# Kernel optimization log

Hardware: AMD Instinct MI355X
Metric: run time of the kernel (lower is better)

The kernel has to match this reference:

```python
import jax, jax.numpy as jnp
import numpy as np

NUM_GENES = 50000
NUM_EDGES = 5000
NNZ = 1_600_000
NUM_PATHWAYS = 500
NUM_TREATMENTS = 20
D = 128        # embed_dim
LATENT = 128   # latent_dim
B, M = 64, 200


def setup_inputs() -> dict:
    key = jax.random.key(0)
    ks = jax.random.split(key, 14)
    gene_ids = jax.random.randint(ks[0], (B, M), 0, NUM_GENES)
    context_ids = jax.random.randint(ks[1], (B,), 0, NUM_TREATMENTS)
    # sparse incidence H (COO): H[row, col] = val, shape [NUM_GENES, NUM_EDGES]
    H_rows = jax.random.randint(ks[2], (NNZ,), 0, NUM_GENES)
    H_cols = jax.random.randint(ks[3], (NNZ,), 0, NUM_EDGES)
    H_vals = jnp.ones((NNZ,), jnp.float32)
    gene_embed = 0.02 * jax.random.normal(ks[4], (NUM_GENES, D), jnp.float32)
    treatment_embed = 0.02 * jax.random.normal(ks[5], (NUM_TREATMENTS, D), jnp.float32)
    gene_pathway = jax.random.bernoulli(ks[6], 0.05, (NUM_GENES, NUM_PATHWAYS)).astype(jnp.float32)
    s = 1.0 / np.sqrt(2 * D)
    W1 = s * jax.random.normal(ks[7], (2 * D, D), jnp.float32)
    b1 = jnp.zeros((D,), jnp.float32)
    W2 = (1.0 / np.sqrt(D)) * jax.random.normal(ks[8], (D,), jnp.float32)
    b2 = jnp.zeros((), jnp.float32)
    latent_W = (1.0 / np.sqrt(D)) * jax.random.normal(ks[9], (D, LATENT), jnp.float32)
    latent_b = jnp.zeros((LATENT,), jnp.float32)
    risk_W = (1.0 / np.sqrt(LATENT)) * jax.random.normal(ks[10], (LATENT,), jnp.float32)
    risk_b = jnp.zeros((), jnp.float32)
    return dict(gene_ids=gene_ids, context_ids=context_ids, H_rows=H_rows, H_cols=H_cols,
                H_vals=H_vals, gene_embed=gene_embed, treatment_embed=treatment_embed,
                gene_pathway=gene_pathway, W1=W1, b1=b1, W2=W2, b2=b2,
                latent_W=latent_W, latent_b=latent_b, risk_W=risk_W, risk_b=risk_b)


def _hyper_prop(E, H_rows, H_cols, H_vals):
    Dv = jax.ops.segment_sum(H_vals, H_rows, num_segments=NUM_GENES)
    De = jax.ops.segment_sum(H_vals, H_cols, num_segments=NUM_EDGES)
    dv = jnp.power(Dv + 1e-6, -0.5)[:, None]   # [V,1]
    de = jnp.power(De + 1e-6, -1.0)[:, None]   # [E,1]
    X = E * dv
    # H^T X : scatter node rows into hyperedges
    HX = jax.ops.segment_sum(H_vals[:, None] * X[H_rows], H_cols, num_segments=NUM_EDGES)
    HX = HX * de
    # H (De^-1 H^T X)
    Xp = jax.ops.segment_sum(H_vals[:, None] * HX[H_cols], H_rows, num_segments=NUM_GENES)
    return Xp * dv


def reference(gene_ids, context_ids, H_rows, H_cols, H_vals, gene_embed, treatment_embed,
              gene_pathway, W1, b1, W2, b2, latent_W, latent_b, risk_W, risk_b):
    E_prop = _hyper_prop(gene_embed, H_rows, H_cols, H_vals)   # [V,D]
    X = E_prop[gene_ids]                                       # [B,M,D]
    ctx = treatment_embed[context_ids]                         # [B,D]
    masks = gene_pathway[gene_ids]                             # [B,M,P]
    pathway_sum = jnp.einsum('bmd,bmp->bpd', X, masks)         # [B,P,D]
    counts = jnp.clip(masks.sum(axis=1), 1.0)[..., None]       # [B,P,1]
    rep = pathway_sum / counts                                 # [B,P,D]
    ctx_exp = jnp.broadcast_to(ctx[:, None, :], (rep.shape[0], NUM_PATHWAYS, D))
    attn_in = jnp.concatenate([rep, ctx_exp], axis=-1)         # [B,P,2D]
    h = jnp.tanh(attn_in @ W1 + b1)                            # [B,P,D]
    scores = h @ W2 + b2                                       # [B,P]
    w = jax.nn.softmax(scores, axis=-1)
    z0 = jnp.einsum('bp,bpd->bd', w, rep)                      # [B,D]
    z = z0 @ latent_W + latent_b                               # [B,LATENT]
    risk = z @ risk_W + risk_b                                 # [B]
    return risk, z
```

## Files before the change

kernel.cpp:

```cpp
#include <hip/hip_runtime.h>
#include <math.h>

#define NGENES 50000
#define NEDGES 5000
#define NNZ_C 1600000
#define NPATH 500
#define DIM 128
#define BB 64
#define MM 200
#define BMN (BB * MM)
#define NBMW 1568
#define CSRCAP 400000
#define NCH 32
#define RNG 12512
#define GSTRIDE 50048
#define NT 8
#define TILESZ 6250
#define NBIN (NT * NEDGES)
#define BIN0 50048
#define EDGE0 90048
#define RED_N 95048
#define SCB_BIN 40
#define SCB_ROW 49
#define SCB (SCB_BIN + SCB_ROW)

__device__ inline float wred_sum(float x) {
#pragma unroll
  for (int off = 32; off > 0; off >>= 1) x += __shfl_down(x, off, 64);
  return x;
}
__device__ inline int wred_sumi(int x) {
#pragma unroll
  for (int off = 32; off > 0; off >>= 1) x += __shfl_down(x, off, 64);
  return x;
}
__device__ inline float wred_max(float x) {
#pragma unroll
  for (int off = 32; off > 0; off >>= 1) x = fmaxf(x, __shfl_down(x, off, 64));
  return x;
}
__device__ inline int wave_incl_scan(int x) {
  int lane = threadIdx.x & 63;
#pragma unroll
  for (int off = 1; off < 64; off <<= 1) {
    int y = __shfl_up(x, off, 64);
    if (lane >= off) x += y;
  }
  return x;
}

__global__ void k_mark(const int* __restrict__ gene_ids, unsigned* __restrict__ bitmap) {
  int i = blockIdx.x * blockDim.x + threadIdx.x;
  if (i >= BMN) return;
  int g = gene_ids[i];
  atomicOr(bitmap + (g >> 5), 1u << (g & 31));
}

__global__ void k_build(const int* __restrict__ rows, const int* __restrict__ cols,
                        const float* __restrict__ vals, const unsigned* __restrict__ bitmap,
                        float* __restrict__ pdv, int* __restrict__ pcnt,
                        int* __restrict__ pbc, float* __restrict__ pde) {
  __shared__ char smem_raw[60000];
  int c = blockIdx.x, role = blockIdx.y, tid = threadIdx.x;
  int lo = c * (NNZ_C / NCH), hi = lo + (NNZ_C / NCH);
  if (role < 4) {
    float* hs = (float*)smem_raw;
    int rlo = role * RNG;
    for (int j = tid; j < RNG; j += 1024) hs[j] = 0.f;
    __syncthreads();
    for (int i = lo + tid; i < hi; i += 1024) {
      int r = rows[i];
      unsigned d = (unsigned)(r - rlo);
      if (d < RNG) atomicAdd(&hs[d], vals[i]);
    }
    __syncthreads();
    float* dst = pdv + (size_t)c * GSTRIDE + rlo;
    for (int j = tid; j < RNG; j += 1024) dst[j] = hs[j];
  } else if (role < 8) {
    int* hs = (int*)smem_raw;
    unsigned* bm = (unsigned*)(smem_raw + RNG * 4);
    int rlo = (role - 4) * RNG;
    for (int j = tid; j < RNG; j += 1024) hs[j] = 0;
    for (int j = tid; j < NBMW; j += 1024) bm[j] = bitmap[j];
    __syncthreads();
    for (int i = lo + tid; i < hi; i += 1024) {
      int r = rows[i];
      unsigned d = (unsigned)(r - rlo);
      if (d < RNG && ((bm[r >> 5] >> (r & 31)) & 1)) atomicAdd(&hs[d], 1);
    }
    __syncthreads();
    int* dst = pcnt + (size_t)c * GSTRIDE + rlo;
    for (int j = tid; j < RNG; j += 1024) dst[j] = hs[j];
  } else {
    int p = role - 8;
    int* hc = (int*)smem_raw;
    float* hs = (float*)(smem_raw + 40000);
    for (int j = tid; j < 2 * NEDGES; j += 1024) hc[j] = 0;
    for (int j = tid; j < NEDGES; j += 1024) hs[j] = 0.f;
    __syncthreads();
    for (int i = lo + tid; i < hi; i += 1024) {
      int r = rows[i];
      int t = r / TILESZ;
      if ((t >> 1) != p) continue;
      int e = cols[i];
      atomicAdd(&hc[(t & 1) * NEDGES + e], 1);
      atomicAdd(&hs[e], vals[i]);
    }
    __syncthreads();
    for (int j = tid; j < 2 * NEDGES; j += 1024) {
      int h = j / NEDGES, e = j - h * NEDGES;
      pbc[(size_t)c * NBIN + (2 * p + h) * NEDGES + e] = hc[j];
    }
    for (int j = tid; j < NEDGES; j += 1024)
      pde[((size_t)c * 4 + p) * NEDGES + j] = hs[j];
  }
}

__global__ void k_reduce(const float* __restrict__ pdv, const int* __restrict__ pcnt,
                         const int* __restrict__ pbc, const float* __restrict__ pde,
                         float* __restrict__ dv_inv, int* __restrict__ row_cnt,
                         int* __restrict__ ccpre8, int* __restrict__ cnt8em,
                         float* __restrict__ de_inv) {
  int idx = blockIdx.x * 256 + threadIdx.x;
  if (idx < NGENES) {
    float s = 0.f;
    int n = 0;
    for (int c = 0; c < NCH; ++c) {
      s += pdv[(size_t)c * GSTRIDE + idx];
      n += pcnt[(size_t)c * GSTRIDE + idx];
    }
    dv_inv[idx] = 1.f / sqrtf(s + 1e-6f);
    row_cnt[idx] = n;
  } else if (idx >= BIN0 && idx < BIN0 + NBIN) {
    int b = idx - BIN0;
    int t = b / NEDGES, e = b - t * NEDGES;
    int run = 0;
    for (int c = 0; c < NCH; ++c) {
      ccpre8[(size_t)c * NBIN + b] = run;
      run += pbc[(size_t)c * NBIN + b];
    }
    cnt8em[(e << 3) | t] = run;
  } else if (idx >= EDGE0 && idx < EDGE0 + NEDGES) {
    int e = idx - EDGE0;
    float s = 0.f;
    for (int cp = 0; cp < NCH * 4; ++cp) s += pde[(size_t)cp * NEDGES + e];
    de_inv[e] = 1.f / (s + 1e-6f);
  }
}

__global__ void k_sc1(const int* __restrict__ cnt8em, const int* __restrict__ row_cnt,
                      int* __restrict__ bsum) {
  __shared__ int wsum[4];
  int blk = blockIdx.x, t = threadIdx.x, lane = t & 63, wid = t >> 6;
  const int* in;
  int base, n;
  if (blk < SCB_BIN) { in = cnt8em; base = blk * 1024; n = NBIN; }
  else { in = row_cnt; base = (blk - SCB_BIN) * 1024; n = NGENES; }
  int s = 0;
#pragma unroll
  for (int k = 0; k < 4; ++k) {
    int e = base + t + k * 256;
    if (e < n) s += in[e];
  }
  s = wred_sumi(s);
  if (lane == 0) wsum[wid] = s;
  __syncthreads();
  if (t == 0) bsum[blk] = wsum[0] + wsum[1] + wsum[2] + wsum[3];
}

__global__ void k_sc2(const int* __restrict__ bsum, int* __restrict__ boff) {
  int t = threadIdx.x, lane = t & 63, wid = t >> 6;
  if (wid == 0) {
    int x = (lane < SCB_BIN) ? bsum[lane] : 0;
    int incl = wave_incl_scan(x);
    if (lane < SCB_BIN) boff[lane] = incl - x;
  } else {
    int x = (lane < SCB_ROW) ? bsum[SCB_BIN + lane] : 0;
    int incl = wave_incl_scan(x);
    if (lane < SCB_ROW) boff[SCB_BIN + lane] = incl - x;
  }
}

__global__ void k_sc3(const int* __restrict__ cnt8em, const int* __restrict__ row_cnt,
                      const int* __restrict__ boff,
                      int* __restrict__ start8, int* __restrict__ row_start) {
  __shared__ int lds[1024];
  __shared__ int wsum[4];
  int blk = blockIdx.x, t = threadIdx.x, lane = t & 63, wid = t >> 6;
  const int* in;
  int* out;
  int base, n;
  if (blk < SCB_BIN) { in = cnt8em; out = start8; base = blk * 1024; n = NBIN; }
  else { in = row_cnt; out = row_start; base = (blk - SCB_BIN) * 1024; n = NGENES; }
  int coff = boff[blk];
#pragma unroll
  for (int k = 0; k < 4; ++k) {
    int e = t + k * 256;
    lds[e] = (base + e < n) ? in[base + e] : 0;
  }
  __syncthreads();
  int x0 = lds[4 * t], x1 = lds[4 * t + 1], x2 = lds[4 * t + 2], x3 = lds[4 * t + 3];
  int s = x0 + x1 + x2 + x3;
  int incl = wave_incl_scan(s);
  if (lane == 63) wsum[wid] = incl;
  __syncthreads();
  int woff = 0;
  for (int w = 0; w < wid; ++w) woff += wsum[w];
  int tb = coff + woff + incl - s;
  int i0 = base + 4 * t;
  if (i0 + 3 < n) {
    ((int4*)(out + i0))[0] = make_int4(tb, tb + x0, tb + x0 + x1, tb + x0 + x1 + x2);
  } else {
    if (i0 < n) out[i0] = tb;
    if (i0 + 1 < n) out[i0 + 1] = tb + x0;
    if (i0 + 2 < n) out[i0 + 2] = tb + x0 + x1;
    if (i0 + 3 < n) out[i0 + 3] = tb + x0 + x1 + x2;
  }
}

__global__ void k_place(const int* __restrict__ rows, const int* __restrict__ cols,
                        const float* __restrict__ vals, const float* __restrict__ dv_inv,
                        const int* __restrict__ start8, const int* __restrict__ ccpre8,
                        const int* __restrict__ row_start, int* __restrict__ row_cur,
                        const unsigned* __restrict__ bitmap,
                        int2* __restrict__ csc, int2* __restrict__ csr) {
  __shared__ char smem_raw[40000];
  int c = blockIdx.x, role = blockIdx.y, tid = threadIdx.x;
  int lo = c * (NNZ_C / NCH), hi = lo + (NNZ_C / NCH);
  if (role < 4) {
    int* cnt_s = (int*)smem_raw;
    for (int j = tid; j < 2 * NEDGES; j += 1024) cnt_s[j] = 0;
    __syncthreads();
    const int* cp = ccpre8 + (size_t)c * NBIN;
    for (int i = lo + tid; i < hi; i += 1024) {
      int r = rows[i];
      int t = r / TILESZ;
      if ((t >> 1) != role) continue;
      int e = cols[i];
      float w = vals[i] * dv_inv[r];
      int rank = atomicAdd(&cnt_s[(t & 1) * NEDGES + e], 1);
      int pos = start8[e * 8 + t] + cp[t * NEDGES + e] + rank;
      csc[pos] = make_int2(r, __float_as_int(w));
    }
  } else {
    unsigned* bm_s = (unsigned*)smem_raw;
    for (int j = tid; j < NBMW; j += 1024) bm_s[j] = bitmap[j];
    __syncthreads();
    for (int i = lo + tid; i < hi; i += 1024) {
      int r = rows[i];
      if ((bm_s[r >> 5] >> (r & 31)) & 1) {
        int p2 = row_start[r] + atomicAdd(row_cur + r, 1);
        if (p2 < CSRCAP) csr[p2] = make_int2(cols[i], __float_as_int(vals[i]));
      }
    }
  }
}

__global__ void k_edge_t(const int* __restrict__ start8, const int* __restrict__ cnt8em,
                         const int2* __restrict__ csc, const float* __restrict__ ge,
                         float* __restrict__ part) {
  __shared__ float4 red[32];
  int bid = blockIdx.x;
  int s = start8[bid];
  int n = cnt8em[bid];
  int g = threadIdx.x >> 5, l = threadIdx.x & 31;
  float4 a0 = make_float4(0.f, 0.f, 0.f, 0.f);
  float4 a1 = make_float4(0.f, 0.f, 0.f, 0.f);
  float4 a2 = make_float4(0.f, 0.f, 0.f, 0.f);
  float4 a3 = make_float4(0.f, 0.f, 0.f, 0.f);
  int i = s + g;
  int end = s + n;
  for (; i + 6 < end; i += 8) {
    int2 e0 = csc[i];
    int2 e1 = csc[i + 2];
    int2 e2 = csc[i + 4];
    int2 e3 = csc[i + 6];
    float4 x0 = *((const float4*)(ge + (size_t)e0.x * DIM) + l);
    float4 x1 = *((const float4*)(ge + (size_t)e1.x * DIM) + l);
    float4 x2 = *((const float4*)(ge + (size_t)e2.x * DIM) + l);
    float4 x3 = *((const float4*)(ge + (size_t)e3.x * DIM) + l);
    float w0 = __int_as_float(e0.y), w1 = __int_as_float(e1.y);
    float w2 = __int_as_float(e2.y), w3 = __int_as_float(e3.y);
    a0.x += w0 * x0.x; a0.y += w0 * x0.y; a0.z += w0 * x0.z; a0.w += w0 * x0.w;
    a1.x += w1 * x1.x; a1.y += w1 * x1.y; a1.z += w1 * x1.z; a1.w += w1 * x1.w;
    a2.x += w2 * x2.x; a2.y += w2 * x2.y; a2.z += w2 * x2.z; a2.w += w2 * x2.w;
    a3.x += w3 * x3.x; a3.y += w3 * x3.y; a3.z += w3 * x3.z; a3.w += w3 * x3.w;
  }
  for (; i < end; i += 2) {
    int2 en = csc[i];
    float w = __int_as_float(en.y);
    float4 x = *((const float4*)(ge + (size_t)en.x * DIM) + l);
    a0.x += w * x.x; a0.y += w * x.y; a0.z += w * x.z; a0.w += w * x.w;
  }
  a0.x += a1.x + a2.x + a3.x;
  a0.y += a1.y + a2.y + a3.y;
  a0.z += a1.z + a2.z + a3.z;
  a0.w += a1.w + a2.w + a3.w;
  if (g == 1) red[l] = a0;
  __syncthreads();
  if (g == 0) {
    float4 b = red[l];
    a0.x += b.x; a0.y += b.y; a0.z += b.z; a0.w += b.w;
    *((float4*)(part + (size_t)bid * DIM) + l) = a0;
  }
}

__global__ void k_edge_red(const float* __restrict__ part, const float* __restrict__ de_inv,
                           float* __restrict__ HXde) {
  int e = blockIdx.x, d = threadIdx.x;
  float s = 0.f;
#pragma unroll
  for (int t = 0; t < NT; ++t) s += part[((size_t)e * 8 + t) * DIM + d];
  HXde[(size_t)e * DIM + d] = s * de_inv[e];
}

__global__ void k_gene(const int* __restrict__ gene_ids, const int* __restrict__ row_start,
                       const int* __restrict__ row_cnt, const int2* __restrict__ csr,
                       const float* __restrict__ HXde, const float* __restrict__ dv_inv,
                       float* __restrict__ Xg) {
  __shared__ float4 red[4][32];
  int bm = blockIdx.x;
  int gene = gene_ids[bm];
  int s = row_start[gene], n = row_cnt[gene];
  int end = s + n;
  int g = threadIdx.x >> 5, l = threadIdx.x & 31;
  float4 a0 = make_float4(0.f, 0.f, 0.f, 0.f);
  float4 a1 = make_float4(0.f, 0.f, 0.f, 0.f);
  int i = s + g;
  for (; i + 4 < end; i += 8) {
    int2 e0 = csr[i];
    int2 e1 = csr[i + 4];
    float4 x0 = *((const float4*)(HXde + (size_t)e0.x * DIM) + l);
    float4 x1 = *((const float4*)(HXde + (size_t)e1.x * DIM) + l);
    float v0 = __int_as_float(e0.y), v1 = __int_as_float(e1.y);
    a0.x += v0 * x0.x; a0.y += v0 * x0.y; a0.z += v0 * x0.z; a0.w += v0 * x0.w;
    a1.x += v1 * x1.x; a1.y += v1 * x1.y; a1.z += v1 * x1.z; a1.w += v1 * x1.w;
  }
  for (; i < end; i += 4) {
    int2 en = csr[i];
    float v = __int_as_float(en.y);
    float4 x = *((const float4*)(HXde + (size_t)en.x * DIM) + l);
    a0.x += v * x.x; a0.y += v * x.y; a0.z += v * x.z; a0.w += v * x.w;
  }
  a0.x += a1.x; a0.y += a1.y; a0.z += a1.z; a0.w += a1.w;
  red[g][l] = a0;
  __syncthreads();
  if (g == 0) {
    float4 a = red[0][l], b = red[1][l], c = red[2][l], d = red[3][l];
    float dvg = dv_inv[gene];
    float4 o;
    o.x = (a.x + b.x + c.x + d.x) * dvg;
    o.y = (a.y + b.y + c.y + d.y) * dvg;
    o.z = (a.z + b.z + c.z + d.z) * dvg;
    o.w = (a.w + b.w + c.w + d.w) * dvg;
    *((float4*)(Xg + (size_t)bm * DIM) + l) = o;
  }
}

#define PT 20
#define CHM 25
__global__ void k_pathway(const int* __restrict__ gene_ids,
                          const float* __restrict__ gene_pathway,
                          const float* __restrict__ Xg, float* __restrict__ rep) {
  __shared__ __align__(16) float buf[2][CHM * PT];
  __shared__ int gid_s[MM];
  int b = blockIdx.y;
  int p0 = blockIdx.x * PT;
  int t = threadIdx.x;
  int d = t;
  if (t < 128) gid_s[t] = gene_ids[b * MM + t];
  if (t + 128 < MM) gid_s[t + 128] = gene_ids[b * MM + t + 128];
  __syncthreads();
  float acc[PT], cnt[PT];
#pragma unroll
  for (int pp = 0; pp < PT; ++pp) { acc[pp] = 0.f; cnt[pp] = 0.f; }
  float r[4];
#pragma unroll
  for (int k = 0; k < 4; ++k) {
    int e = t + k * 128;
    if (e < CHM * PT) {
      int ml = e / PT, po = e - ml * PT;
      r[k] = gene_pathway[(size_t)gid_s[ml] * NPATH + p0 + po];
    }
  }
  const float* Xb = Xg + (size_t)b * MM * DIM + d;
  for (int ch = 0; ch < MM / CHM; ++ch) {
    float* bw = buf[ch & 1];
#pragma unroll
    for (int k = 0; k < 4; ++k) {
      int e = t + k * 128;
      if (e < CHM * PT) bw[e] = r[k];
    }
    __syncthreads();
    if (ch + 1 < MM / CHM) {
      int m0n = (ch + 1) * CHM;
#pragma unroll
      for (int k = 0; k < 4; ++k) {
        int e = t + k * 128;
        if (e < CHM * PT) {
          int ml = e / PT, po = e - ml * PT;
          r[k] = gene_pathway[(size_t)gid_s[m0n + ml] * NPATH + p0 + po];
        }
      }
    }
    const float* br = buf[ch & 1];
    int m0 = ch * CHM;
    for (int ml = 0; ml < CHM; ++ml) {
      float x = Xb[(size_t)(m0 + ml) * DIM];
      const float4* mr = (const float4*)(br + ml * PT);
#pragma unroll
      for (int q = 0; q < 5; ++q) {
        float4 v = mr[q];
        acc[4 * q + 0] += v.x * x; cnt[4 * q + 0] += v.x;
        acc[4 * q + 1] += v.y * x; cnt[4 * q + 1] += v.y;
        acc[4 * q + 2] += v.z * x; cnt[4 * q + 2] += v.z;
        acc[4 * q + 3] += v.w * x; cnt[4 * q + 3] += v.w;
      }
    }
  }
#pragma unroll
  for (int pp = 0; pp < PT; ++pp) {
    rep[((size_t)b * NPATH + p0 + pp) * DIM + d] = acc[pp] / fmaxf(cnt[pp], 1.f);
  }
}

#define PT2 10
__global__ void k_attn(const float* __restrict__ rep, const int* __restrict__ context_ids,
                       const float* __restrict__ treatment_embed,
                       const float* __restrict__ W1, const float* __restrict__ b1,
                       const float* __restrict__ W2, const float* __restrict__ b2,
                       float* __restrict__ scores) {
  __shared__ float in_s[PT2][DIM];
  __shared__ float ctx_s[DIM];
  __shared__ float part[PT2][2];
  int b = blockIdx.y;
  int p0 = blockIdx.x * PT2;
  int j = threadIdx.x;
  int lane = j & 63, wid = j >> 6;
  ctx_s[j] = treatment_embed[context_ids[b] * DIM + j];
#pragma unroll
  for (int pp = 0; pp < PT2; ++pp)
    in_s[pp][j] = rep[((size_t)b * NPATH + p0 + pp) * DIM + j];
  __syncthreads();
  float base = b1[j];
  for (int k = 0; k < DIM; ++k) base += ctx_s[k] * W1[(DIM + k) * DIM + j];
  float acc[PT2];
#pragma unroll
  for (int pp = 0; pp < PT2; ++pp) acc[pp] = base;
  for (int k = 0; k < DIM; ++k) {
    float w1 = W1[k * DIM + j];
#pragma unroll
    for (int pp = 0; pp < PT2; ++pp) acc[pp] += in_s[pp][k] * w1;
  }
  float w2 = W2[j];
#pragma unroll
  for (int pp = 0; pp < PT2; ++pp) {
    float t = tanhf(acc[pp]) * w2;
    t = wred_sum(t);
    if (lane == 0) part[pp][wid] = t;
  }
  __syncthreads();
  if (j < PT2) scores[b * NPATH + p0 + j] = part[j][0] + part[j][1] + b2[0];
}

__global__ void k_final(const float* __restrict__ scores, const float* __restrict__ rep,
                        const float* __restrict__ latent_W, const float* __restrict__ latent_b,
                        const float* __restrict__ risk_W, const float* __restrict__ risk_b,
                        float* __restrict__ out) {
  __shared__ float w_s[NPATH];
  __shared__ float z0_s[DIM];
  __shared__ float red_max[2], red_sum[2], red_risk[2];
  int b = blockIdx.x, t = threadIdx.x;
  int lane = t & 63, wid = t >> 6;
  float lmax = -3.4e38f;
  for (int p = t; p < NPATH; p += 128) {
    float s = scores[b * NPATH + p];
    w_s[p] = s;
    lmax = fmaxf(lmax, s);
  }
  lmax = wred_max(lmax);
  if (lane == 0) red_max[wid] = lmax;
  __syncthreads();
  float bmax = fmaxf(red_max[0], red_max[1]);
  float lsum = 0.f;
  for (int p = t; p < NPATH; p += 128) {
    float e = expf(w_s[p] - bmax);
    w_s[p] = e;
    lsum += e;
  }
  lsum = wred_sum(lsum);
  if (lane == 0) red_sum[wid] = lsum;
  __syncthreads();
  float inv = 1.f / (red_sum[0] + red_sum[1]);
  int d = t;
  const float* repb = rep + (size_t)b * NPATH * DIM + d;
  float z00 = 0.f, z01 = 0.f, z02 = 0.f, z03 = 0.f;
  for (int p = 0; p < NPATH; p += 4) {
    z00 += w_s[p] * repb[(size_t)p * DIM];
    z01 += w_s[p + 1] * repb[(size_t)(p + 1) * DIM];
    z02 += w_s[p + 2] * repb[(size_t)(p + 2) * DIM];
    z03 += w_s[p + 3] * repb[(size_t)(p + 3) * DIM];
  }
  float z0 = ((z00 + z01) + (z02 + z03)) * inv;
  z0_s[d] = z0;
  __syncthreads();
  float z = latent_b[t];
  for (int dd = 0; dd < DIM; ++dd) z += z0_s[dd] * latent_W[dd * DIM + t];
  out[BB + b * DIM + t] = z;
  float r = z * risk_W[t];
  r = wred_sum(r);
  if (lane == 0) red_risk[wid] = r;
  __syncthreads();
  if (t == 0) out[b] = red_risk[0] + red_risk[1] + risk_b[0];
}

extern "C" void kernel_launch(void* const* d_in, const int* in_sizes, int n_in,
                              void* d_out, int out_size, void* d_ws, size_t ws_size,
                              hipStream_t stream) {
  const int* gene_ids = (const int*)d_in[0];
  const int* context_ids = (const int*)d_in[1];
  const int* H_rows = (const int*)d_in[2];
  const int* H_cols = (const int*)d_in[3];
  const float* H_vals = (const float*)d_in[4];
  const float* gene_embed = (const float*)d_in[5];
  const float* treatment_embed = (const float*)d_in[6];
  const float* gene_pathway = (const float*)d_in[7];
  const float* W1 = (const float*)d_in[8];
  const float* b1 = (const float*)d_in[9];
  const float* W2 = (const float*)d_in[10];
  const float* b2 = (const float*)d_in[11];
  const float* latent_W = (const float*)d_in[12];
  const float* latent_b = (const float*)d_in[13];
  const float* risk_W = (const float*)d_in[14];
  const float* risk_b = (const float*)d_in[15];
  float* out = (float*)d_out;

  char* ws = (char*)d_ws;
  float* dv_inv = (float*)(ws + 0);
  float* de_inv = (float*)(ws + 200000);
  int* row_cnt = (int*)(ws + 220000);
  int* row_start = (int*)(ws + 420000);
  int* cnt8em = (int*)(ws + 620000);
  int* start8 = (int*)(ws + 780000);
  int* ccpre8 = (int*)(ws + 940000);
  float* scores = (float*)(ws + 6060000);
  int* bsum = (int*)(ws + 6220800);
  int* boff = (int*)(ws + 6221312);
  int* row_cur = (int*)(ws + 6349824);
  unsigned* bitmap = (unsigned*)(ws + 6549824);
  int2* csc = (int2*)(ws + 6556096);
  int2* csr = (int2*)(ws + 19356096);
  float* HXde = (float*)(ws + 22556096);
  float* part = (float*)(ws + 25116096);
  float* pdv = (float*)(ws + 6556096);
  int* pcnt = (int*)(ws + 12962240);
  int* pbc = (int*)(ws + 19368384);
  float* pde = (float*)(ws + 24488384);
  float* Xg = (float*)(ws + 25116096);
  float* rep = (float*)(ws + 31669696);

  hipMemsetAsync(ws + 6349824, 0, 206272, stream);

  k_mark<<<(BMN + 255) / 256, 256, 0, stream>>>(gene_ids, bitmap);
  k_build<<<dim3(NCH, 12), 1024, 0, stream>>>(H_rows, H_cols, H_vals, bitmap,
                                              pdv, pcnt, pbc, pde);
  k_reduce<<<(RED_N + 255) / 256, 256, 0, stream>>>(pdv, pcnt, pbc, pde, dv_inv, row_cnt,
                                                    ccpre8, cnt8em, de_inv);
  k_sc1<<<SCB, 256, 0, stream>>>(cnt8em, row_cnt, bsum);
  k_sc2<<<1, 128, 0, stream>>>(bsum, boff);
  k_sc3<<<SCB, 256, 0, stream>>>(cnt8em, row_cnt, boff, start8, row_start);
  k_place<<<dim3(NCH, 5), 1024, 0, stream>>>(H_rows, H_cols, H_vals, dv_inv,
                                             start8, ccpre8, row_start, row_cur,
                                             bitmap, csc, csr);
  k_edge_t<<<NBIN, 64, 0, stream>>>(start8, cnt8em, csc, gene_embed, part);
  k_edge_red<<<NEDGES, DIM, 0, stream>>>(part, de_inv, HXde);
  k_gene<<<BMN, 128, 0, stream>>>(gene_ids, row_start, row_cnt, csr, HXde, dv_inv, Xg);
  k_pathway<<<dim3(NPATH / PT, BB), DIM, 0, stream>>>(gene_ids, gene_pathway, Xg, rep);
  k_attn<<<dim3(NPATH / PT2, BB), DIM, 0, stream>>>(rep, context_ids, treatment_embed,
                                                    W1, b1, W2, b2, scores);
  k_final<<<BB, DIM, 0, stream>>>(scores, rep, latent_W, latent_b, risk_W, risk_b, out);
}
```

Before: 501.7 us.

## Replace chunked shared-memory histograms with direct global atomics for CSR/CSC build

Replaces the per-chunk shared-memory histogram build and the per-chunk prefix reduction with a single pass that does global atomic adds for degree sums, bin counts and row counts. Placement now uses global atomic cursors per bin and per row instead of deterministic chunk prefixes. This removes the large partial buffers and their reduction traffic, and shrinks the workspace. In exchange it adds heavy global atomic contention (about 1.6M atomics on 5000 edge sums) and makes the order of entries within a bin, and so the float summation order, nondeterministic.

```diff
diff --git a/kernel.cpp b/kernel.cpp
--- a/kernel.cpp
+++ b/kernel.cpp
@@ -11,15 +11,9 @@
 #define BMN (BB * MM)
 #define NBMW 1568
 #define CSRCAP 400000
-#define NCH 32
-#define RNG 12512
-#define GSTRIDE 50048
 #define NT 8
 #define TILESZ 6250
 #define NBIN (NT * NEDGES)
-#define BIN0 50048
-#define EDGE0 90048
-#define RED_N 95048
 #define SCB_BIN 40
 #define SCB_ROW 49
 #define SCB (SCB_BIN + SCB_ROW)
@@ -56,95 +50,29 @@
   atomicOr(bitmap + (g >> 5), 1u << (g & 31));
 }
 
-__global__ void k_build(const int* __restrict__ rows, const int* __restrict__ cols,
-                        const float* __restrict__ vals, const unsigned* __restrict__ bitmap,
-                        float* __restrict__ pdv, int* __restrict__ pcnt,
-                        int* __restrict__ pbc, float* __restrict__ pde) {
-  __shared__ char smem_raw[60000];
-  int c = blockIdx.x, role = blockIdx.y, tid = threadIdx.x;
-  int lo = c * (NNZ_C / NCH), hi = lo + (NNZ_C / NCH);
-  if (role < 4) {
-    float* hs = (float*)smem_raw;
-    int rlo = role * RNG;
-    for (int j = tid; j < RNG; j += 1024) hs[j] = 0.f;
-    __syncthreads();
-    for (int i = lo + tid; i < hi; i += 1024) {
-      int r = rows[i];
-      unsigned d = (unsigned)(r - rlo);
-      if (d < RNG) atomicAdd(&hs[d], vals[i]);
-    }
-    __syncthreads();
-    float* dst = pdv + (size_t)c * GSTRIDE + rlo;
-    for (int j = tid; j < RNG; j += 1024) dst[j] = hs[j];
-  } else if (role < 8) {
-    int* hs = (int*)smem_raw;
-    unsigned* bm = (unsigned*)(smem_raw + RNG * 4);
-    int rlo = (role - 4) * RNG;
-    for (int j = tid; j < RNG; j += 1024) hs[j] = 0;
-    for (int j = tid; j < NBMW; j += 1024) bm[j] = bitmap[j];
-    __syncthreads();
-    for (int i = lo + tid; i < hi; i += 1024) {
-      int r = rows[i];
-      unsigned d = (unsigned)(r - rlo);
-      if (d < RNG && ((bm[r >> 5] >> (r & 31)) & 1)) atomicAdd(&hs[d], 1);
-    }
-    __syncthreads();
-    int* dst = pcnt + (size_t)c * GSTRIDE + rlo;
-    for (int j = tid; j < RNG; j += 1024) dst[j] = hs[j];
-  } else {
-    int p = role - 8;
-    int* hc = (int*)smem_raw;
-    float* hs = (float*)(smem_raw + 40000);
-    for (int j = tid; j < 2 * NEDGES; j += 1024) hc[j] = 0;
-    for (int j = tid; j < NEDGES; j += 1024) hs[j] = 0.f;
-    __syncthreads();
-    for (int i = lo + tid; i < hi; i += 1024) {
-      int r = rows[i];
-      int t = r / TILESZ;
-      if ((t >> 1) != p) continue;
-      int e = cols[i];
-      atomicAdd(&hc[(t & 1) * NEDGES + e], 1);
-      atomicAdd(&hs[e], vals[i]);
-    }
-    __syncthreads();
-    for (int j = tid; j < 2 * NEDGES; j += 1024) {
-      int h = j / NEDGES, e = j - h * NEDGES;
-      pbc[(size_t)c * NBIN + (2 * p + h) * NEDGES + e] = hc[j];
-    }
-    for (int j = tid; j < NEDGES; j += 1024)
-      pde[((size_t)c * 4 + p) * NEDGES + j] = hs[j];
-  }
-}
-
-__global__ void k_reduce(const float* __restrict__ pdv, const int* __restrict__ pcnt,
-                         const int* __restrict__ pbc, const float* __restrict__ pde,
-                         float* __restrict__ dv_inv, int* __restrict__ row_cnt,
-                         int* __restrict__ ccpre8, int* __restrict__ cnt8em,
-                         float* __restrict__ de_inv) {
-  int idx = blockIdx.x * 256 + threadIdx.x;
-  if (idx < NGENES) {
-    float s = 0.f;
-    int n = 0;
-    for (int c = 0; c < NCH; ++c) {
-      s += pdv[(size_t)c * GSTRIDE + idx];
-      n += pcnt[(size_t)c * GSTRIDE + idx];
-    }
-    dv_inv[idx] = 1.f / sqrtf(s + 1e-6f);
-    row_cnt[idx] = n;
-  } else if (idx >= BIN0 && idx < BIN0 + NBIN) {
-    int b = idx - BIN0;
-    int t = b / NEDGES, e = b - t * NEDGES;
-    int run = 0;
-    for (int c = 0; c < NCH; ++c) {
-      ccpre8[(size_t)c * NBIN + b] = run;
-      run += pbc[(size_t)c * NBIN + b];
-    }
-    cnt8em[(e << 3) | t] = run;
-  } else if (idx >= EDGE0 && idx < EDGE0 + NEDGES) {
-    int e = idx - EDGE0;
-    float s = 0.f;
-    for (int cp = 0; cp < NCH * 4; ++cp) s += pde[(size_t)cp * NEDGES + e];
-    de_inv[e] = 1.f / (s + 1e-6f);
+__global__ void k_hist(const int* __restrict__ rows, const int* __restrict__ cols,
+                       const float* __restrict__ vals, const unsigned* __restrict__ bitmap,
+                       float* __restrict__ dv_sum, float* __restrict__ de_sum,
+                       int* __restrict__ cnt8em, int* __restrict__ row_cnt) {
+  int i = blockIdx.x * 256 + threadIdx.x;
+  if (i >= NNZ_C) return;
+  int r = rows[i];
+  int e = cols[i];
+  float v = vals[i];
+  atomicAdd(dv_sum + r, v);
+  atomicAdd(de_sum + e, v);
+  atomicAdd(cnt8em + ((e << 3) | (r / TILESZ)), 1);
+  if ((bitmap[r >> 5] >> (r & 31)) & 1) atomicAdd(row_cnt + r, 1);
+}
+
+__global__ void k_reduce2(const float* __restrict__ dv_sum, const float* __restrict__ de_sum,
+                          float* __restrict__ dv_inv, float* __restrict__ de_inv) {
+  int i = blockIdx.x * 256 + threadIdx.x;
+  if (i < NGENES) {
+    dv_inv[i] = 1.f / sqrtf(dv_sum[i] + 1e-6f);
+  } else if (i < NGENES + NEDGES) {
+    int e = i - NGENES;
+    de_inv[e] = 1.f / (de_sum[e] + 1e-6f);
   }
 }
 
@@ -218,41 +146,24 @@
   }
 }
 
-__global__ void k_place(const int* __restrict__ rows, const int* __restrict__ cols,
-                        const float* __restrict__ vals, const float* __restrict__ dv_inv,
-                        const int* __restrict__ start8, const int* __restrict__ ccpre8,
-                        const int* __restrict__ row_start, int* __restrict__ row_cur,
-                        const unsigned* __restrict__ bitmap,
-                        int2* __restrict__ csc, int2* __restrict__ csr) {
-  __shared__ char smem_raw[40000];
-  int c = blockIdx.x, role = blockIdx.y, tid = threadIdx.x;
-  int lo = c * (NNZ_C / NCH), hi = lo + (NNZ_C / NCH);
-  if (role < 4) {
-    int* cnt_s = (int*)smem_raw;
-    for (int j = tid; j < 2 * NEDGES; j += 1024) cnt_s[j] = 0;
-    __syncthreads();
-    const int* cp = ccpre8 + (size_t)c * NBIN;
-    for (int i = lo + tid; i < hi; i += 1024) {
-      int r = rows[i];
-      int t = r / TILESZ;
-      if ((t >> 1) != role) continue;
-      int e = cols[i];
-      float w = vals[i] * dv_inv[r];
-      int rank = atomicAdd(&cnt_s[(t & 1) * NEDGES + e], 1);
-      int pos = start8[e * 8 + t] + cp[t * NEDGES + e] + rank;
-      csc[pos] = make_int2(r, __float_as_int(w));
-    }
-  } else {
-    unsigned* bm_s = (unsigned*)smem_raw;
-    for (int j = tid; j < NBMW; j += 1024) bm_s[j] = bitmap[j];
-    __syncthreads();
-    for (int i = lo + tid; i < hi; i += 1024) {
-      int r = rows[i];
-      if ((bm_s[r >> 5] >> (r & 31)) & 1) {
-        int p2 = row_start[r] + atomicAdd(row_cur + r, 1);
-        if (p2 < CSRCAP) csr[p2] = make_int2(cols[i], __float_as_int(vals[i]));
-      }
-    }
+__global__ void k_place2(const int* __restrict__ rows, const int* __restrict__ cols,
+                         const float* __restrict__ vals, const float* __restrict__ dv_inv,
+                         const int* __restrict__ start8, const int* __restrict__ row_start,
+                         const unsigned* __restrict__ bitmap,
+                         int* __restrict__ bin_cur, int* __restrict__ row_cur,
+                         int2* __restrict__ csc, int2* __restrict__ csr) {
+  int i = blockIdx.x * 256 + threadIdx.x;
+  if (i >= NNZ_C) return;
+  int r = rows[i];
+  int e = cols[i];
+  float v = vals[i];
+  int bin = (e << 3) | (r / TILESZ);
+  float w = v * dv_inv[r];
+  int pos = start8[bin] + atomicAdd(bin_cur + bin, 1);
+  csc[pos] = make_int2(r, __float_as_int(w));
+  if ((bitmap[r >> 5] >> (r & 31)) & 1) {
+    int p2 = row_start[r] + atomicAdd(row_cur + r, 1);
+    if (p2 < CSRCAP) csr[p2] = make_int2(e, __float_as_int(v));
   }
 }
 
@@ -538,40 +449,38 @@
   char* ws = (char*)d_ws;
   float* dv_inv = (float*)(ws + 0);
   float* de_inv = (float*)(ws + 200000);
-  int* row_cnt = (int*)(ws + 220000);
-  int* row_start = (int*)(ws + 420000);
-  int* cnt8em = (int*)(ws + 620000);
-  int* start8 = (int*)(ws + 780000);
-  int* ccpre8 = (int*)(ws + 940000);
-  float* scores = (float*)(ws + 6060000);
-  int* bsum = (int*)(ws + 6220800);
-  int* boff = (int*)(ws + 6221312);
-  int* row_cur = (int*)(ws + 6349824);
-  unsigned* bitmap = (unsigned*)(ws + 6549824);
-  int2* csc = (int2*)(ws + 6556096);
-  int2* csr = (int2*)(ws + 19356096);
-  float* HXde = (float*)(ws + 22556096);
-  float* part = (float*)(ws + 25116096);
-  float* pdv = (float*)(ws + 6556096);
-  int* pcnt = (int*)(ws + 12962240);
-  int* pbc = (int*)(ws + 19368384);
-  float* pde = (float*)(ws + 24488384);
-  float* Xg = (float*)(ws + 25116096);
-  float* rep = (float*)(ws + 31669696);
-
-  hipMemsetAsync(ws + 6349824, 0, 206272, stream);
+  int* row_start = (int*)(ws + 220000);
+  int* start8 = (int*)(ws + 420000);
+  float* scores = (float*)(ws + 580000);
+  int* bsum = (int*)(ws + 708000);
+  int* boff = (int*)(ws + 708416);
+  int* row_cnt = (int*)(ws + 708800);
+  int* row_cur = (int*)(ws + 908800);
+  float* dv_sum = (float*)(ws + 1108800);
+  float* de_sum = (float*)(ws + 1308800);
+  int* cnt8em = (int*)(ws + 1328800);
+  int* bin_cur = (int*)(ws + 1488800);
+  unsigned* bitmap = (unsigned*)(ws + 1648800);
+  int2* csc = (int2*)(ws + 1655104);
+  int2* csr = (int2*)(ws + 14455104);
+  float* HXde = (float*)(ws + 17655104);
+  float* part = (float*)(ws + 20215104);
+  float* Xg = (float*)(ws + 20215104);
+  float* rep = (float*)(ws + 26768704);
+
+  hipMemsetAsync(ws + 708800, 0, 946272, stream);
 
   k_mark<<<(BMN + 255) / 256, 256, 0, stream>>>(gene_ids, bitmap);
-  k_build<<<dim3(NCH, 12), 1024, 0, stream>>>(H_rows, H_cols, H_vals, bitmap,
-                                              pdv, pcnt, pbc, pde);
-  k_reduce<<<(RED_N + 255) / 256, 256, 0, stream>>>(pdv, pcnt, pbc, pde, dv_inv, row_cnt,
-                                                    ccpre8, cnt8em, de_inv);
+  k_hist<<<NNZ_C / 256, 256, 0, stream>>>(H_rows, H_cols, H_vals, bitmap,
+                                          dv_sum, de_sum, cnt8em, row_cnt);
+  k_reduce2<<<(NGENES + NEDGES + 255) / 256, 256, 0, stream>>>(dv_sum, de_sum,
+                                                               dv_inv, de_inv);
   k_sc1<<<SCB, 256, 0, stream>>>(cnt8em, row_cnt, bsum);
   k_sc2<<<1, 128, 0, stream>>>(bsum, boff);
   k_sc3<<<SCB, 256, 0, stream>>>(cnt8em, row_cnt, boff, start8, row_start);
-  k_place<<<dim3(NCH, 5), 1024, 0, stream>>>(H_rows, H_cols, H_vals, dv_inv,
-                                             start8, ccpre8, row_start, row_cur,
-                                             bitmap, csc, csr);
+  k_place2<<<NNZ_C / 256, 256, 0, stream>>>(H_rows, H_cols, H_vals, dv_inv,
+                                            start8, row_start, bitmap,
+                                            bin_cur, row_cur, csc, csr);
   k_edge_t<<<NBIN, 64, 0, stream>>>(start8, cnt8em, csc, gene_embed, part);
   k_edge_red<<<NEDGES, DIM, 0, stream>>>(part, de_inv, HXde);
   k_gene<<<BMN, 128, 0, stream>>>(gene_ids, row_start, row_cnt, csr, HXde, dv_inv, Xg);
```

Result: slower. 734.3 us (+46.4%).

## Double build chunks, pack 16-bit histogram counters, merge CSR placement into CSC roles

Applied to the files above, without the earlier changes.

Raises the number of nnz chunks from 32 to 64 and packs two 16-bit counters per shared-memory int in the build histograms. This halves the count and bin roles, so k_build needs 8 roles instead of 12 and each role scans the input fewer times. The partial count arrays become unsigned short to cut workspace traffic. k_place drops its separate CSR role and does CSR placement inside the four row-tile CSC roles, so the nnz stream is read fewer times overall. The risks are 16-bit overflow if per-chunk counts grow, and more atomics per thread in the merged placement loop.

```diff
diff --git a/kernel.cpp b/kernel.cpp
--- a/kernel.cpp
+++ b/kernel.cpp
@@ -11,7 +11,7 @@
 #define BMN (BB * MM)
 #define NBMW 1568
 #define CSRCAP 400000
-#define NCH 32
+#define NCH 64
 #define RNG 12512
 #define GSTRIDE 50048
 #define NT 8
@@ -58,9 +58,9 @@
 
 __global__ void k_build(const int* __restrict__ rows, const int* __restrict__ cols,
                         const float* __restrict__ vals, const unsigned* __restrict__ bitmap,
-                        float* __restrict__ pdv, int* __restrict__ pcnt,
-                        int* __restrict__ pbc, float* __restrict__ pde) {
-  __shared__ char smem_raw[60000];
+                        float* __restrict__ pdv, unsigned short* __restrict__ pcnt,
+                        unsigned short* __restrict__ pbc, float* __restrict__ pde) {
+  __shared__ char smem_raw[60032];
   int c = blockIdx.x, role = blockIdx.y, tid = threadIdx.x;
   int lo = c * (NNZ_C / NCH), hi = lo + (NNZ_C / NCH);
   if (role < 4) {
@@ -76,50 +76,63 @@
     __syncthreads();
     float* dst = pdv + (size_t)c * GSTRIDE + rlo;
     for (int j = tid; j < RNG; j += 1024) dst[j] = hs[j];
-  } else if (role < 8) {
+  } else if (role < 6) {
     int* hs = (int*)smem_raw;
     unsigned* bm = (unsigned*)(smem_raw + RNG * 4);
-    int rlo = (role - 4) * RNG;
+    int q = role - 4;
+    int qlo = q * (2 * RNG);
     for (int j = tid; j < RNG; j += 1024) hs[j] = 0;
     for (int j = tid; j < NBMW; j += 1024) bm[j] = bitmap[j];
     __syncthreads();
     for (int i = lo + tid; i < hi; i += 1024) {
       int r = rows[i];
-      unsigned d = (unsigned)(r - rlo);
-      if (d < RNG && ((bm[r >> 5] >> (r & 31)) & 1)) atomicAdd(&hs[d], 1);
-    }
-    __syncthreads();
-    int* dst = pcnt + (size_t)c * GSTRIDE + rlo;
-    for (int j = tid; j < RNG; j += 1024) dst[j] = hs[j];
+      unsigned d = (unsigned)(r - qlo);
+      if (d < 2u * RNG && ((bm[r >> 5] >> (r & 31)) & 1)) {
+        int half = d >= (unsigned)RNG;
+        atomicAdd(&hs[half ? (int)d - RNG : (int)d], 1 << (half * 16));
+      }
+    }
+    __syncthreads();
+    unsigned short* dst = pcnt + (size_t)c * GSTRIDE + qlo;
+    for (int j = tid; j < RNG; j += 1024) {
+      unsigned v = (unsigned)hs[j];
+      dst[j] = (unsigned short)(v & 0xFFFFu);
+      dst[j + RNG] = (unsigned short)(v >> 16);
+    }
   } else {
-    int p = role - 8;
-    int* hc = (int*)smem_raw;
-    float* hs = (float*)(smem_raw + 40000);
-    for (int j = tid; j < 2 * NEDGES; j += 1024) hc[j] = 0;
-    for (int j = tid; j < NEDGES; j += 1024) hs[j] = 0.f;
-    __syncthreads();
+    int q = role - 6;
+    int* hcp = (int*)smem_raw;
+    float* hsde = (float*)(smem_raw + 40000);
+    for (int j = tid; j < 2 * NEDGES; j += 1024) hcp[j] = 0;
+    for (int j = tid; j < NEDGES; j += 1024) hsde[j] = 0.f;
+    __syncthreads();
+    int tlo = q * 4;
     for (int i = lo + tid; i < hi; i += 1024) {
       int r = rows[i];
       int t = r / TILESZ;
-      if ((t >> 1) != p) continue;
+      unsigned u = (unsigned)(t - tlo);
+      if (u >= 4u) continue;
       int e = cols[i];
-      atomicAdd(&hc[(t & 1) * NEDGES + e], 1);
-      atomicAdd(&hs[e], vals[i]);
+      atomicAdd(&hcp[(u >> 1) * NEDGES + e], 1 << ((u & 1) * 16));
+      atomicAdd(&hsde[e], vals[i]);
     }
     __syncthreads();
     for (int j = tid; j < 2 * NEDGES; j += 1024) {
       int h = j / NEDGES, e = j - h * NEDGES;
-      pbc[(size_t)c * NBIN + (2 * p + h) * NEDGES + e] = hc[j];
+      unsigned v = (unsigned)hcp[j];
+      int t0 = tlo + 2 * h;
+      pbc[(size_t)c * NBIN + (size_t)t0 * NEDGES + e] = (unsigned short)(v & 0xFFFFu);
+      pbc[(size_t)c * NBIN + (size_t)(t0 + 1) * NEDGES + e] = (unsigned short)(v >> 16);
     }
     for (int j = tid; j < NEDGES; j += 1024)
-      pde[((size_t)c * 4 + p) * NEDGES + j] = hs[j];
-  }
-}
-
-__global__ void k_reduce(const float* __restrict__ pdv, const int* __restrict__ pcnt,
-                         const int* __restrict__ pbc, const float* __restrict__ pde,
+      pde[((size_t)c * 2 + q) * NEDGES + j] = hsde[j];
+  }
+}
+
+__global__ void k_reduce(const float* __restrict__ pdv, const unsigned short* __restrict__ pcnt,
+                         const unsigned short* __restrict__ pbc, const float* __restrict__ pde,
                          float* __restrict__ dv_inv, int* __restrict__ row_cnt,
-                         int* __restrict__ ccpre8, int* __restrict__ cnt8em,
+                         unsigned short* __restrict__ ccpre8, int* __restrict__ cnt8em,
                          float* __restrict__ de_inv) {
   int idx = blockIdx.x * 256 + threadIdx.x;
   if (idx < NGENES) {
@@ -136,14 +149,14 @@
     int t = b / NEDGES, e = b - t * NEDGES;
     int run = 0;
     for (int c = 0; c < NCH; ++c) {
-      ccpre8[(size_t)c * NBIN + b] = run;
+      ccpre8[(size_t)c * NBIN + b] = (unsigned short)run;
       run += pbc[(size_t)c * NBIN + b];
     }
     cnt8em[(e << 3) | t] = run;
   } else if (idx >= EDGE0 && idx < EDGE0 + NEDGES) {
     int e = idx - EDGE0;
     float s = 0.f;
-    for (int cp = 0; cp < NCH * 4; ++cp) s += pde[(size_t)cp * NEDGES + e];
+    for (int cp = 0; cp < NCH * 2; ++cp) s += pde[(size_t)cp * NEDGES + e];
     de_inv[e] = 1.f / (s + 1e-6f);
   }
 }
@@ -220,38 +233,34 @@
 
 __global__ void k_place(const int* __restrict__ rows, const int* __restrict__ cols,
                         const float* __restrict__ vals, const float* __restrict__ dv_inv,
-                        const int* __restrict__ start8, const int* __restrict__ ccpre8,
+                        const int* __restrict__ start8, const unsigned short* __restrict__ ccpre8,
                         const int* __restrict__ row_start, int* __restrict__ row_cur,
                         const unsigned* __restrict__ bitmap,
                         int2* __restrict__ csc, int2* __restrict__ csr) {
-  __shared__ char smem_raw[40000];
+  __shared__ int cnt_s[2 * NEDGES];
+  __shared__ unsigned bm_s[NBMW];
   int c = blockIdx.x, role = blockIdx.y, tid = threadIdx.x;
   int lo = c * (NNZ_C / NCH), hi = lo + (NNZ_C / NCH);
-  if (role < 4) {
-    int* cnt_s = (int*)smem_raw;
-    for (int j = tid; j < 2 * NEDGES; j += 1024) cnt_s[j] = 0;
-    __syncthreads();
-    const int* cp = ccpre8 + (size_t)c * NBIN;
-    for (int i = lo + tid; i < hi; i += 1024) {
-      int r = rows[i];
-      int t = r / TILESZ;
-      if ((t >> 1) != role) continue;
-      int e = cols[i];
-      float w = vals[i] * dv_inv[r];
-      int rank = atomicAdd(&cnt_s[(t & 1) * NEDGES + e], 1);
-      int pos = start8[e * 8 + t] + cp[t * NEDGES + e] + rank;
-      csc[pos] = make_int2(r, __float_as_int(w));
-    }
-  } else {
-    unsigned* bm_s = (unsigned*)smem_raw;
-    for (int j = tid; j < NBMW; j += 1024) bm_s[j] = bitmap[j];
-    __syncthreads();
-    for (int i = lo + tid; i < hi; i += 1024) {
-      int r = rows[i];
-      if ((bm_s[r >> 5] >> (r & 31)) & 1) {
-        int p2 = row_start[r] + atomicAdd(row_cur + r, 1);
-        if (p2 < CSRCAP) csr[p2] = make_int2(cols[i], __float_as_int(vals[i]));
-      }
+  for (int j = tid; j < 2 * NEDGES; j += 1024) cnt_s[j] = 0;
+  for (int j = tid; j < NBMW; j += 1024) bm_s[j] = bitmap[j];
+  __syncthreads();
+  const unsigned short* cp = ccpre8 + (size_t)c * NBIN;
+  int rlo = role * (2 * TILESZ);
+  for (int i = lo + tid; i < hi; i += 1024) {
+    int r = rows[i];
+    unsigned d = (unsigned)(r - rlo);
+    if (d >= 2u * TILESZ) continue;
+    int e = cols[i];
+    float v = vals[i];
+    int thi = d >= (unsigned)TILESZ;
+    int t = 2 * role + thi;
+    float w = v * dv_inv[r];
+    int rank = atomicAdd(&cnt_s[thi * NEDGES + e], 1);
+    int pos = start8[e * 8 + t] + (int)cp[(size_t)t * NEDGES + e] + rank;
+    csc[pos] = make_int2(r, __float_as_int(w));
+    if ((bm_s[r >> 5] >> (r & 31)) & 1) {
+      int p2 = row_start[r] + atomicAdd(row_cur + r, 1);
+      if (p2 < CSRCAP) csr[p2] = make_int2(e, __float_as_int(v));
     }
   }
 }
@@ -542,34 +551,34 @@
   int* row_start = (int*)(ws + 420000);
   int* cnt8em = (int*)(ws + 620000);
   int* start8 = (int*)(ws + 780000);
-  int* ccpre8 = (int*)(ws + 940000);
+  unsigned short* ccpre8 = (unsigned short*)(ws + 940000);
   float* scores = (float*)(ws + 6060000);
-  int* bsum = (int*)(ws + 6220800);
-  int* boff = (int*)(ws + 6221312);
-  int* row_cur = (int*)(ws + 6349824);
-  unsigned* bitmap = (unsigned*)(ws + 6549824);
-  int2* csc = (int2*)(ws + 6556096);
-  int2* csr = (int2*)(ws + 19356096);
-  float* HXde = (float*)(ws + 22556096);
-  float* part = (float*)(ws + 25116096);
-  float* pdv = (float*)(ws + 6556096);
-  int* pcnt = (int*)(ws + 12962240);
-  int* pbc = (int*)(ws + 19368384);
-  float* pde = (float*)(ws + 24488384);
-  float* Xg = (float*)(ws + 25116096);
-  float* rep = (float*)(ws + 31669696);
-
-  hipMemsetAsync(ws + 6349824, 0, 206272, stream);
+  int* bsum = (int*)(ws + 6188032);
+  int* boff = (int*)(ws + 6188544);
+  int* row_cur = (int*)(ws + 6189056);
+  unsigned* bitmap = (unsigned*)(ws + 6389056);
+  int2* csc = (int2*)(ws + 6395328);
+  int2* csr = (int2*)(ws + 19195328);
+  float* HXde = (float*)(ws + 22395328);
+  float* part = (float*)(ws + 24955328);
+  float* pdv = (float*)(ws + 6395328);
+  unsigned short* pcnt = (unsigned short*)(ws + 19207616);
+  unsigned short* pbc = (unsigned short*)(ws + 25613760);
+  float* pde = (float*)(ws + 30733760);
+  float* Xg = (float*)(ws + 24955328);
+  float* rep = (float*)(ws + 31508928);
+
+  hipMemsetAsync(ws + 6189056, 0, 206272, stream);
 
   k_mark<<<(BMN + 255) / 256, 256, 0, stream>>>(gene_ids, bitmap);
-  k_build<<<dim3(NCH, 12), 1024, 0, stream>>>(H_rows, H_cols, H_vals, bitmap,
-                                              pdv, pcnt, pbc, pde);
+  k_build<<<dim3(NCH, 8), 1024, 0, stream>>>(H_rows, H_cols, H_vals, bitmap,
+                                             pdv, pcnt, pbc, pde);
   k_reduce<<<(RED_N + 255) / 256, 256, 0, stream>>>(pdv, pcnt, pbc, pde, dv_inv, row_cnt,
                                                     ccpre8, cnt8em, de_inv);
   k_sc1<<<SCB, 256, 0, stream>>>(cnt8em, row_cnt, bsum);
   k_sc2<<<1, 128, 0, stream>>>(bsum, boff);
   k_sc3<<<SCB, 256, 0, stream>>>(cnt8em, row_cnt, boff, start8, row_start);
-  k_place<<<dim3(NCH, 5), 1024, 0, stream>>>(H_rows, H_cols, H_vals, dv_inv,
+  k_place<<<dim3(NCH, 4), 1024, 0, stream>>>(H_rows, H_cols, H_vals, dv_inv,
                                              start8, ccpre8, row_start, row_cur,
                                              bitmap, csc, csr);
   k_edge_t<<<NBIN, 64, 0, stream>>>(start8, cnt8em, csc, gene_embed, part);
```

Result: faster. 460.0 us (-8.3%).
